# Optimization experiments

Hardware: AMD Instinct MI355X
Metric: run time of the kernel (lower is better)

The kernel has to match this reference:

```python
import jax, jax.numpy as jnp
import numpy as np

C = 512
C8 = C // 8


def setup_inputs() -> dict:
    key = jax.random.key(0)
    ks = jax.random.split(key, 7)
    B, W = 8, 2048
    x = jax.random.normal(ks[0], (B, C, W), dtype=jnp.float32)
    # 1x1 Conv1d == pointwise linear: weight [out, in], bias [out]
    s_q = 1.0 / np.sqrt(C)
    Wq = jax.random.uniform(ks[1], (C8, C), jnp.float32, -s_q, s_q)
    bq = jax.random.uniform(ks[2], (C8,), jnp.float32, -s_q, s_q)
    Wk = jax.random.uniform(ks[3], (C8, C), jnp.float32, -s_q, s_q)
    bk = jax.random.uniform(ks[4], (C8,), jnp.float32, -s_q, s_q)
    Wv = jax.random.uniform(ks[5], (C, C), jnp.float32, -s_q, s_q)
    bv = jax.random.uniform(ks[6], (C,), jnp.float32, -s_q, s_q)
    gamma = jnp.zeros((1,), dtype=jnp.float32)
    return {"x": x, "Wq": Wq, "bq": bq, "Wk": Wk, "bk": bk, "Wv": Wv, "bv": bv, "gamma": gamma}


def reference(x, Wq, bq, Wk, bk, Wv, bv, gamma):
    # x: [B, C, W]; 1x1 conv projections (pointwise linear over channel dim)
    q = jnp.einsum('oc,bcw->bwo', Wq, x) + bq            # [B, W, C/8]
    k = jnp.einsum('oc,bcw->bow', Wk, x) + bk[:, None]   # [B, C/8, W]
    v = jnp.einsum('oc,bcw->bow', Wv, x) + bv[:, None]   # [B, C, W]
    # attention[b, i, j] over keys j (no scaling, matching the original)
    attn = jax.nn.softmax(jnp.einsum('bwo,bov->bwv', q, k), axis=-1)  # [B, W, W]
    out = jnp.einsum('bcj,bij->bci', v, attn)            # [B, C, W]
    return gamma[0] * out + x
```

## Files before the change

kernel.cpp:

```cpp
#include <hip/hip_runtime.h>
#include <stdint.h>

#define B_  8
#define C_  512
#define CO_ 64
#define W_  2048
#define R_  640
#define LOG2E 1.4426950408889634f

typedef float f32x4 __attribute__((ext_vector_type(4)));
typedef float f32x16 __attribute__((ext_vector_type(16)));
typedef __bf16 bf16x8 __attribute__((ext_vector_type(8)));
typedef __bf16 bf16x2 __attribute__((ext_vector_type(2)));
typedef unsigned u32x2 __attribute__((ext_vector_type(2)));
typedef unsigned u32x4 __attribute__((ext_vector_type(4)));
typedef unsigned short u16;
typedef u16 u16x8 __attribute__((ext_vector_type(8)));
typedef u16 u16x4 __attribute__((ext_vector_type(4)));

static __device__ __forceinline__ float exp2g(float f){
  return __builtin_amdgcn_exp2f(f);
}
static __device__ __forceinline__ u16 f2b(float f){
  union { float f; unsigned u; } v; v.f = f;
  unsigned r = v.u + 0x7FFFu + ((v.u >> 16) & 1u);
  return (u16)(r >> 16);
}
static __device__ __forceinline__ bf16x8 ldb(const u16* p){
  return __builtin_bit_cast(bf16x8, *(const u16x8*)p);
}
static __device__ __forceinline__ f32x4 mfma16(bf16x8 a, bf16x8 b, f32x4 c){
  return __builtin_amdgcn_mfma_f32_16x16x32_bf16(a, b, c, 0, 0, 0);
}
static __device__ __forceinline__ f32x16 mfma32(bf16x8 a, bf16x8 b, f32x16 c){
  return __builtin_amdgcn_mfma_f32_32x32x16_bf16(a, b, c, 0, 0, 0);
}
static __device__ __forceinline__ void pl32swap(unsigned &a, unsigned &b){
  asm("v_permlane32_swap_b32 %0, %1" : "+v"(a), "+v"(b));
}
static __device__ __forceinline__ float red_sum32(float v){
  unsigned a = __builtin_bit_cast(unsigned, v), b = a;
  pl32swap(a, b);
  return __builtin_bit_cast(float, a) + __builtin_bit_cast(float, b);
}
static __device__ __forceinline__ unsigned pkbf(float lo, float hi){
  bf16x2 t; t[0] = (__bf16)lo; t[1] = (__bf16)hi;
  return __builtin_bit_cast(unsigned, t);
}
static __device__ __forceinline__ void barrier_lds_only(){
  asm volatile("s_waitcnt lgkmcnt(0)" ::: "memory");
  __builtin_amdgcn_s_barrier();
}

__global__ __launch_bounds__(256) void prep_w(
    const float* __restrict__ Wq, const float* __restrict__ bq,
    const float* __restrict__ Wk, const float* __restrict__ bk,
    const float* __restrict__ Wv, const float* __restrict__ bv,
    u16* __restrict__ af, float* __restrict__ ball){
  int e = blockIdx.x * 256 + threadIdx.x;
  if (e < R_ * C_){
    int r = e >> 9, c = e & (C_ - 1);
    float w;
    if (r < 64)       w = Wq[r * C_ + c] * LOG2E;
    else if (r < 128) w = Wk[(r - 64) * C_ + c];
    else              w = Wv[(r - 128) * C_ + c];
    int mt16 = r >> 4, mr = r & 15;
    int kk = c >> 5, g = (c >> 3) & 3, e8 = c & 7;
    af[(((size_t)mt16 * 16 + kk) * 64 + g * 16 + mr) * 8 + e8] = f2b(w);
  }
  if (e < R_){
    float bb;
    if (e < 64)       bb = bq[e] * LOG2E;
    else if (e < 128) bb = bk[e - 64];
    else              bb = bv[e - 128];
    ball[e] = bb;
  }
}

#define PADB 520
__global__ __launch_bounds__(512) void gemm_fused(
    const u16* __restrict__ af, const float* __restrict__ ball,
    const float* __restrict__ x, u16* __restrict__ qf,
    u16* __restrict__ kf, u16* __restrict__ vf){
  __shared__ u16 bt[64][PADB];
  __shared__ float t[32][65];
  int b = blockIdx.y;
  int w0 = blockIdx.x * 64;
  int tid = threadIdx.x, lane = tid & 63, wid = tid >> 6;
  int ws = wid >> 2, wm = (wid >> 1) & 1, wn = wid & 1;
  int g = lane >> 4, r = lane & 15;
  const float* xb = x + (size_t)b * C_ * W_;

  {
    int rrow = tid >> 4, wseg = (tid & 15) * 4;
    int tw = tid >> 3, cseg = (tid & 7) * 4;
    for (int cc = 0; cc < 16; cc++){
      const float* xp = &xb[(size_t)(cc * 32 + rrow) * W_ + w0 + wseg];
      float v0 = xp[0], v1 = xp[1], v2 = xp[2], v3 = xp[3];
      t[rrow][wseg + 0] = v0; t[rrow][wseg + 1] = v1;
      t[rrow][wseg + 2] = v2; t[rrow][wseg + 3] = v3;
      barrier_lds_only();
      u16x4 pk;
      #pragma unroll
      for (int k = 0; k < 4; k++) pk[k] = f2b(t[cseg + k][tw]);
      *(u16x4*)&bt[tw][cc * 32 + cseg] = pk;
      barrier_lds_only();
    }
  }

  for (int mt = ws; mt < 10; mt += 2){
    f32x4 acc[2][2] = {};
    int mt0 = mt * 4 + wm * 2;
    const u16* ap0 = af + ((size_t)(mt0 * 16) * 64 + lane) * 8;
    const u16* ap1 = af + ((size_t)((mt0 + 1) * 16) * 64 + lane) * 8;
    bf16x8 aX0 = ldb(ap0), aX1 = ldb(ap1);
    bf16x8 aY0, aY1;
    #pragma unroll
    for (int kk = 0; kk < 16; kk += 2){
      aY0 = ldb(ap0 + (kk + 1) * 512);
      aY1 = ldb(ap1 + (kk + 1) * 512);
      {
        bf16x8 b0 = ldb(&bt[wn * 32 +  0 + r][kk * 32 + g * 8]);
        bf16x8 b1 = ldb(&bt[wn * 32 + 16 + r][kk * 32 + g * 8]);
        acc[0][0] = mfma16(aX0, b0, acc[0][0]);
        acc[0][1] = mfma16(aX0, b1, acc[0][1]);
        acc[1][0] = mfma16(aX1, b0, acc[1][0]);
        acc[1][1] = mfma16(aX1, b1, acc[1][1]);
      }
      if (kk + 2 < 16){
        aX0 = ldb(ap0 + (kk + 2) * 512);
        aX1 = ldb(ap1 + (kk + 2) * 512);
      }
      {
        bf16x8 b0 = ldb(&bt[wn * 32 +  0 + r][(kk + 1) * 32 + g * 8]);
        bf16x8 b1 = ldb(&bt[wn * 32 + 16 + r][(kk + 1) * 32 + g * 8]);
        acc[0][0] = mfma16(aY0, b0, acc[0][0]);
        acc[0][1] = mfma16(aY0, b1, acc[0][1]);
        acc[1][0] = mfma16(aY1, b0, acc[1][0]);
        acc[1][1] = mfma16(aY1, b1, acc[1][1]);
      }
    }
    #pragma unroll
    for (int i = 0; i < 2; i++){
      #pragma unroll
      for (int n = 0; n < 2; n++){
        int rbase = mt * 64 + wm * 32 + i * 16 + g * 4;
        int wcol  = w0 + wn * 32 + n * 16 + r;
        if (mt < 2){
          u16* base = (mt == 0 ? qf : kf) + (size_t)b * W_ * CO_;
          int o0 = (rbase & 63);
          int oc = o0 >> 4, h2 = (o0 >> 3) & 1, e0 = o0 & 7;
          u16x4 pk;
          #pragma unroll
          for (int tt = 0; tt < 4; tt++) pk[tt] = f2b(acc[i][n][tt] + ball[rbase + tt]);
          *(u16x4*)&base[((size_t)((wcol >> 5) * 4 + oc) * 64 + h2 * 32 + (wcol & 31)) * 8 + e0] = pk;
        } else {
          u16* vb = vf + (size_t)b * C_ * W_;
          int jt = wcol >> 4, h2 = (wcol >> 3) & 1, e = wcol & 7;
          #pragma unroll
          for (int tt = 0; tt < 4; tt++){
            int c = rbase + tt - 128;
            vb[((size_t)((c >> 5) * (W_ / 16) + jt) * 64 + h2 * 32 + (c & 31)) * 8 + e] =
                f2b(acc[i][n][tt] + ball[rbase + tt]);
          }
        }
      }
    }
  }
}

__global__ __launch_bounds__(512, 2) void attn14(
    const u16* __restrict__ qf, const u16* __restrict__ kf,
    const u16* __restrict__ vf, const float* __restrict__ x,
    const float* __restrict__ gamma, float* __restrict__ out){
  __shared__ u16 pb[2][2][32][132];
  __shared__ float lredf[2][4][32];
  int tid = threadIdx.x, lane = tid & 63, wv = tid >> 6;
  int jw = wv & 3, iw = wv >> 2;
  int bid = blockIdx.x;
  int b = bid & 7;
  int i0 = (bid >> 3) * 64;
  int cbase = wv * 64;
  int li = lane & 31, hi = lane >> 5;
  int swz = (li & 7) << 3;
  const u16* qfb = qf + (size_t)b * W_ * CO_;
  const u16* kfb = kf + (size_t)b * W_ * CO_;
  const u16* vfb = vf + (size_t)b * C_ * W_;

  bf16x8 fq[4];
  {
    const u16* qp = &qfb[(size_t)((i0 >> 5) + iw) * 4 * 512 + lane * 8];
    #pragma unroll
    for (int oc = 0; oc < 4; oc++) fq[oc] = ldb(qp + oc * 512);
  }

  const u16* kp = &kfb[(size_t)jw * 2048 + lane * 8];
  const u16* vpt0 = &vfb[(size_t)(cbase >> 5) * (W_ / 16) * 512 + lane * 8];
  const u16* vpt1 = vpt0 + (size_t)(W_ / 16) * 512;

  f32x16 acc00 = {}, acc01 = {}, acc10 = {}, acc11 = {};
  f32x4 lacc = {};

  auto sphase = [&](bf16x8 (&fk)[4], int bsel){
    f32x16 S = {};
    S = mfma32(fk[0], fq[0], S);
    S = mfma32(fk[1], fq[1], S);
    S = mfma32(fk[2], fq[2], S);
    S = mfma32(fk[3], fq[3], S);
    float p[16];
    #pragma unroll
    for (int t = 0; t < 16; t++) p[t] = exp2g(S[t]);
    #pragma unroll
    for (int t = 0; t < 4; t++)
      lacc[t] += ((p[t] + p[4 + t]) + (p[8 + t] + p[12 + t]));
    #pragma unroll
    for (int B = 0; B < 4; B++){
      unsigned lo = pkbf(p[4 * B + 0], p[4 * B + 1]);
      unsigned h2 = pkbf(p[4 * B + 2], p[4 * B + 3]);
      int j0 = (jw * 32 + 8 * B + 4 * hi) ^ swz;
      u32x2 wpair = {lo, h2};
      *(u32x2*)&pb[bsel][iw][li][j0] = wpair;
    }
  };
  auto pfrag = [&](int bsel, int it, int jj, int kj) -> bf16x8 {
    int j0 = (jj * 32 + kj * 16 + 8 * hi) ^ swz;
    u16x4 a = *(const u16x4*)&pb[bsel][it][li][j0];
    u16x4 c = *(const u16x4*)&pb[bsel][it][li][j0 + 4];
    u16x8 w = {a[0], a[1], a[2], a[3], c[0], c[1], c[2], c[3]};
    return __builtin_bit_cast(bf16x8, w);
  };
  auto loadV = [&](bf16x8 (&fv)[4], int off){
    fv[0] = ldb(vpt0 + off); fv[1] = ldb(vpt0 + off + 512);
    fv[2] = ldb(vpt1 + off); fv[3] = ldb(vpt1 + off + 512);
  };
  auto PV = [&](bf16x8 (&fv)[4], int bsel, int jj){
    bf16x8 p00 = pfrag(bsel, 0, jj, 0), p01 = pfrag(bsel, 0, jj, 1);
    bf16x8 p10 = pfrag(bsel, 1, jj, 0), p11 = pfrag(bsel, 1, jj, 1);
    __builtin_amdgcn_s_setprio(1);
    acc00 = mfma32(fv[0], p00, acc00); acc00 = mfma32(fv[1], p01, acc00);
    acc10 = mfma32(fv[2], p00, acc10); acc10 = mfma32(fv[3], p01, acc10);
    acc01 = mfma32(fv[0], p10, acc01); acc01 = mfma32(fv[1], p11, acc01);
    acc11 = mfma32(fv[2], p10, acc11); acc11 = mfma32(fv[3], p11, acc11);
    __builtin_amdgcn_s_setprio(0);
  };

  bf16x8 fvX[4], fvY[4];
  {
    bf16x8 fk[4];
    #pragma unroll
    for (int oc = 0; oc < 4; oc++) fk[oc] = ldb(kp + oc * 512);
    sphase(fk, 0);
  }
  loadV(fvX, 0);
  barrier_lds_only();

  int cur = 0;
  for (int m = 0; m < 16; ++m){
    bf16x8 fkN[4];
    if (m < 15){
      const u16* kpn = kp + 8192;
      #pragma unroll
      for (int oc = 0; oc < 4; oc++) fkN[oc] = ldb(kpn + oc * 512);
    }
    loadV(fvY, 1024);
    PV(fvX, cur, 0);
    loadV(fvX, 2048);
    PV(fvY, cur, 1);
    loadV(fvY, 3072);
    PV(fvX, cur, 2);
    if (m < 15) loadV(fvX, 4096);
    PV(fvY, cur, 3);
    if (m < 15) sphase(fkN, cur ^ 1);
    kp += 8192; vpt0 += 4096; vpt1 += 4096;
    barrier_lds_only();
    cur ^= 1;
  }

  float l = (lacc[0] + lacc[1]) + (lacc[2] + lacc[3]);
  l = red_sum32(l);
  if (hi == 0) lredf[iw][jw][li] = l;
  __syncthreads();
  float lf0 = (lredf[0][0][li] + lredf[0][1][li]) + (lredf[0][2][li] + lredf[0][3][li]);
  float lf1 = (lredf[1][0][li] + lredf[1][1][li]) + (lredf[1][2][li] + lredf[1][3][li]);

  float gm = gamma[0];
  float iv0 = 1.f / lf0, iv1 = 1.f / lf1;
  const float* xb = x + (size_t)b * C_ * W_;
  float* ob = out + (size_t)b * C_ * W_;
  auto epi = [&](f32x16 &acc, int ct, int it, float iv){
    int icol = i0 + it * 32 + li;
    #pragma unroll
    for (int t = 0; t < 16; t++){
      int crow = (t & 3) + 8 * (t >> 2) + 4 * hi;
      int c = cbase + ct * 32 + crow;
      ob[(size_t)c * W_ + icol] = gm * (acc[t] * iv) + xb[(size_t)c * W_ + icol];
    }
  };
  epi(acc00, 0, 0, iv0); epi(acc10, 1, 0, iv0);
  epi(acc01, 0, 1, iv1); epi(acc11, 1, 1, iv1);
}

extern "C" void kernel_launch(void* const* d_in, const int* in_sizes, int n_in,
                              void* d_out, int out_size, void* d_ws, size_t ws_size,
                              hipStream_t stream) {
  const float* x     = (const float*)d_in[0];
  const float* Wq    = (const float*)d_in[1];
  const float* bq    = (const float*)d_in[2];
  const float* Wk    = (const float*)d_in[3];
  const float* bk    = (const float*)d_in[4];
  const float* Wv    = (const float*)d_in[5];
  const float* bv    = (const float*)d_in[6];
  const float* gamma = (const float*)d_in[7];
  float* out = (float*)d_out;
  char* ws = (char*)d_ws;
  u16*   af   = (u16*)  (ws + 0);
  float* ball = (float*)(ws + 655360);
  u16*   qf   = (u16*)  (ws + 17435136);
  u16*   kf   = (u16*)  (ws + 19532288);
  u16*   vf   = (u16*)  (ws + 21629440);

  prep_w<<<dim3(1280), dim3(256), 0, stream>>>(Wq, bq, Wk, bk, Wv, bv, af, ball);
  gemm_fused<<<dim3(32, 8), dim3(512), 0, stream>>>(af, ball, x, qf, kf, vf);
  attn14<<<dim3(256), dim3(512), 0, stream>>>(qf, kf, vf, x, gamma, out);
}
```

Baseline: 90.13 us.

## Pipeline projection GEMM loads and stage V output through LDS for vector stores

The fused projection GEMM now double-buffers the x transpose tile and prefetches x rows several chunks ahead. It also keeps eight k-steps of A fragments in registers and prefetches the next M tile's fragments during the current tile's MFMAs. The V output is transposed through a new LDS buffer so each lane writes 16-byte vectors instead of scattered 2-byte stores. This aims to hide global load latency and cut uncoalesced writes, at the cost of more registers and LDS plus extra barriers per V tile.

```diff
diff --git a/kernel.cpp b/kernel.cpp
--- a/kernel.cpp
+++ b/kernel.cpp
@@ -83,7 +83,8 @@
     const float* __restrict__ x, u16* __restrict__ qf,
     u16* __restrict__ kf, u16* __restrict__ vf){
   __shared__ u16 bt[64][PADB];
-  __shared__ float t[32][65];
+  __shared__ float t[2][32][65];
+  __shared__ u16 vt[2][64][68];
   int b = blockIdx.y;
   int w0 = blockIdx.x * 64;
   int tid = threadIdx.x, lane = tid & 63, wid = tid >> 6;
@@ -91,80 +92,113 @@
   int g = lane >> 4, r = lane & 15;
   const float* xb = x + (size_t)b * C_ * W_;
 
+  const u16* apc0 = af + ((size_t)((ws * 4 + wm * 2) * 16) * 64 + lane) * 8;
+  const u16* apc1 = apc0 + 8192;
+  bf16x8 a[8][2];
+  #pragma unroll
+  for (int k = 0; k < 8; k++){
+    a[k][0] = ldb(apc0 + k * 512);
+    a[k][1] = ldb(apc1 + k * 512);
+  }
+
   {
     int rrow = tid >> 4, wseg = (tid & 15) * 4;
     int tw = tid >> 3, cseg = (tid & 7) * 4;
-    for (int cc = 0; cc < 16; cc++){
-      const float* xp = &xb[(size_t)(cc * 32 + rrow) * W_ + w0 + wseg];
-      float v0 = xp[0], v1 = xp[1], v2 = xp[2], v3 = xp[3];
-      t[rrow][wseg + 0] = v0; t[rrow][wseg + 1] = v1;
-      t[rrow][wseg + 2] = v2; t[rrow][wseg + 3] = v3;
-      barrier_lds_only();
+    auto ldx = [&](int cc) -> f32x4 {
+      return *(const f32x4*)&xb[(size_t)(cc * 32 + rrow) * W_ + w0 + wseg];
+    };
+    auto st_t = [&](int buf, f32x4 v){
+      t[buf][rrow][wseg + 0] = v[0]; t[buf][rrow][wseg + 1] = v[1];
+      t[buf][rrow][wseg + 2] = v[2]; t[buf][rrow][wseg + 3] = v[3];
+    };
+    auto rd_bt = [&](int cc, int buf){
       u16x4 pk;
       #pragma unroll
-      for (int k = 0; k < 4; k++) pk[k] = f2b(t[cseg + k][tw]);
+      for (int k = 0; k < 4; k++) pk[k] = f2b(t[buf][cseg + k][tw]);
       *(u16x4*)&bt[tw][cc * 32 + cseg] = pk;
+    };
+    f32x4 v[4];
+    #pragma unroll
+    for (int k = 0; k < 4; k++) v[k] = ldx(k);
+    st_t(0, v[0]);
+    v[0] = ldx(4);
+    barrier_lds_only();
+    #pragma unroll
+    for (int p = 0; p < 16; p++){
+      rd_bt(p, p & 1);
+      if (p < 15) st_t((p + 1) & 1, v[(p + 1) & 3]);
+      if (p + 5 < 16) v[(p + 1) & 3] = ldx(p + 5);
       barrier_lds_only();
     }
   }
 
   for (int mt = ws; mt < 10; mt += 2){
+    int mtn = (mt + 2 < 10) ? mt + 2 : ws;
+    const u16* apn0 = af + ((size_t)((mtn * 4 + wm * 2) * 16) * 64 + lane) * 8;
+    const u16* apn1 = apn0 + 8192;
     f32x4 acc[2][2] = {};
-    int mt0 = mt * 4 + wm * 2;
-    const u16* ap0 = af + ((size_t)(mt0 * 16) * 64 + lane) * 8;
-    const u16* ap1 = af + ((size_t)((mt0 + 1) * 16) * 64 + lane) * 8;
-    bf16x8 aX0 = ldb(ap0), aX1 = ldb(ap1);
-    bf16x8 aY0, aY1;
-    #pragma unroll
-    for (int kk = 0; kk < 16; kk += 2){
-      aY0 = ldb(ap0 + (kk + 1) * 512);
-      aY1 = ldb(ap1 + (kk + 1) * 512);
-      {
-        bf16x8 b0 = ldb(&bt[wn * 32 +  0 + r][kk * 32 + g * 8]);
-        bf16x8 b1 = ldb(&bt[wn * 32 + 16 + r][kk * 32 + g * 8]);
-        acc[0][0] = mfma16(aX0, b0, acc[0][0]);
-        acc[0][1] = mfma16(aX0, b1, acc[0][1]);
-        acc[1][0] = mfma16(aX1, b0, acc[1][0]);
-        acc[1][1] = mfma16(aX1, b1, acc[1][1]);
+    #pragma unroll
+    for (int kk = 0; kk < 16; kk++){
+      bf16x8 b0 = ldb(&bt[wn * 32 +  0 + r][kk * 32 + g * 8]);
+      bf16x8 b1 = ldb(&bt[wn * 32 + 16 + r][kk * 32 + g * 8]);
+      acc[0][0] = mfma16(a[kk & 7][0], b0, acc[0][0]);
+      acc[0][1] = mfma16(a[kk & 7][0], b1, acc[0][1]);
+      acc[1][0] = mfma16(a[kk & 7][1], b0, acc[1][0]);
+      acc[1][1] = mfma16(a[kk & 7][1], b1, acc[1][1]);
+      if (kk < 8){
+        a[kk][0] = ldb(apc0 + (kk + 8) * 512);
+        a[kk][1] = ldb(apc1 + (kk + 8) * 512);
+      } else {
+        a[kk - 8][0] = ldb(apn0 + (kk - 8) * 512);
+        a[kk - 8][1] = ldb(apn1 + (kk - 8) * 512);
       }
-      if (kk + 2 < 16){
-        aX0 = ldb(ap0 + (kk + 2) * 512);
-        aX1 = ldb(ap1 + (kk + 2) * 512);
-      }
-      {
-        bf16x8 b0 = ldb(&bt[wn * 32 +  0 + r][(kk + 1) * 32 + g * 8]);
-        bf16x8 b1 = ldb(&bt[wn * 32 + 16 + r][(kk + 1) * 32 + g * 8]);
-        acc[0][0] = mfma16(aY0, b0, acc[0][0]);
-        acc[0][1] = mfma16(aY0, b1, acc[0][1]);
-        acc[1][0] = mfma16(aY1, b0, acc[1][0]);
-        acc[1][1] = mfma16(aY1, b1, acc[1][1]);
-      }
-    }
-    #pragma unroll
-    for (int i = 0; i < 2; i++){
+    }
+    apc0 = apn0; apc1 = apn1;
+
+    if (mt < 2){
+      u16* base = (mt == 0 ? qf : kf) + (size_t)b * W_ * CO_;
       #pragma unroll
-      for (int n = 0; n < 2; n++){
-        int rbase = mt * 64 + wm * 32 + i * 16 + g * 4;
-        int wcol  = w0 + wn * 32 + n * 16 + r;
-        if (mt < 2){
-          u16* base = (mt == 0 ? qf : kf) + (size_t)b * W_ * CO_;
+      for (int i = 0; i < 2; i++){
+        #pragma unroll
+        for (int n = 0; n < 2; n++){
+          int rbase = mt * 64 + wm * 32 + i * 16 + g * 4;
+          int wcol  = w0 + wn * 32 + n * 16 + r;
           int o0 = (rbase & 63);
           int oc = o0 >> 4, h2 = (o0 >> 3) & 1, e0 = o0 & 7;
           u16x4 pk;
           #pragma unroll
           for (int tt = 0; tt < 4; tt++) pk[tt] = f2b(acc[i][n][tt] + ball[rbase + tt]);
           *(u16x4*)&base[((size_t)((wcol >> 5) * 4 + oc) * 64 + h2 * 32 + (wcol & 31)) * 8 + e0] = pk;
-        } else {
-          u16* vb = vf + (size_t)b * C_ * W_;
-          int jt = wcol >> 4, h2 = (wcol >> 3) & 1, e = wcol & 7;
-          #pragma unroll
-          for (int tt = 0; tt < 4; tt++){
-            int c = rbase + tt - 128;
-            vb[((size_t)((c >> 5) * (W_ / 16) + jt) * 64 + h2 * 32 + (c & 31)) * 8 + e] =
-                f2b(acc[i][n][tt] + ball[rbase + tt]);
-          }
         }
       }
+    } else {
+      #pragma unroll
+      for (int i = 0; i < 2; i++){
+        #pragma unroll
+        for (int n = 0; n < 2; n++){
+          int cT = wm * 32 + i * 16 + g * 4;
+          int wT = wn * 32 + n * 16 + r;
+          int rb = mt * 64 + cT;
+          #pragma unroll
+          for (int tt = 0; tt < 4; tt++)
+            vt[ws][cT + tt][wT] = f2b(acc[i][n][tt] + ball[rb + tt]);
+        }
+      }
+      barrier_lds_only();
+      {
+        int jt = wid & 3;
+        int h2 = lane >> 5, li = lane & 31;
+        u16* vfb_ = vf + (size_t)b * C_ * W_;
+        #pragma unroll
+        for (int cg = 0; cg < 2; cg++){
+          u16x4 lo = *(const u16x4*)&vt[ws][cg * 32 + li][jt * 16 + h2 * 8];
+          u16x4 hi4 = *(const u16x4*)&vt[ws][cg * 32 + li][jt * 16 + h2 * 8 + 4];
+          u16x8 val = {lo[0], lo[1], lo[2], lo[3], hi4[0], hi4[1], hi4[2], hi4[3]};
+          size_t off = ((size_t)(((mt - 2) * 2 + cg) * (W_ / 16) + (w0 >> 4) + jt) * 64 + lane) * 8;
+          *(u16x8*)&vfb_[off] = val;
+        }
+      }
+      barrier_lds_only();
     }
   }
 }
```

After: 84.84 us. 5.9% less time.
